# Performance work log

Measured on AMD Instinct MI355X. Metric: run time of the kernel, lower is better.

The kernel has to match this reference:

```python
import jax, jax.numpy as jnp
import numpy as np

B, T, RES, C = 4, 8, 32, 128
TSP, SPLIT = 4, 4
NH_BRANCH = 4  # num_heads // 2 per branch
HID = 4 * C


def layer_norm(x, w, b, eps=1e-5):
    mu = x.mean(-1, keepdims=True)
    var = ((x - mu) ** 2).mean(-1, keepdims=True)
    return (x - mu) * jax.lax.rsqrt(var + eps) * w + b


def dwconv3d(x, w, b):
    # x: (Bw, C, Tsp, Hsp, Wsp); w: (C, 1, 3, 3, 3) depthwise
    y = jax.lax.conv_general_dilated(
        x, w, (1, 1, 1), 'SAME',
        dimension_numbers=('NCDHW', 'OIDHW', 'NCDHW'),
        feature_group_count=x.shape[1])
    return y + b[None, :, None, None, None]


def lepe_attention(q, k, v, conv_w, conv_b, Tsp, Hsp, Wsp, nh, Tt, H, W):
    Bq, L, Cc = q.shape
    hd = Cc // nh
    win = Tsp * Hsp * Wsp
    scale = float(hd) ** -0.5

    def to_win(z):
        z = z.reshape(Bq, Tt // Tsp, Tsp, H // Hsp, Hsp, W // Wsp, Wsp, Cc)
        z = z.transpose(0, 1, 3, 5, 2, 4, 6, 7).reshape(-1, win, nh, hd)
        return z.transpose(0, 2, 1, 3)

    qw = to_win(q) * scale
    kw = to_win(k)
    # v windows as (Bw, C, Tsp, Hsp, Wsp) for the depthwise-conv LePE
    vw5 = v.reshape(Bq, Tt // Tsp, Tsp, H // Hsp, Hsp, W // Wsp, Wsp, Cc)
    vw5 = vw5.transpose(0, 1, 3, 5, 7, 2, 4, 6).reshape(-1, Cc, Tsp, Hsp, Wsp)
    lepe = dwconv3d(vw5, conv_w, conv_b)

    def heads(z5):
        return z5.reshape(-1, nh, hd, win).transpose(0, 1, 3, 2)

    vh, lepeh = heads(vw5), heads(lepe)
    attn = jax.nn.softmax(jnp.einsum('bnqd,bnkd->bnqk', qw, kw), axis=-1)
    out = jnp.einsum('bnqk,bnkd->bnqd', attn, vh) + lepeh
    # windows -> video token order (T, H, W)
    out = out.transpose(0, 2, 1, 3).reshape(
        Bq, Tt // Tsp, H // Hsp, W // Wsp, Tsp, Hsp, Wsp, Cc)
    out = out.transpose(0, 1, 4, 2, 5, 3, 6, 7).reshape(Bq, L, Cc)
    return out


def setup_inputs() -> dict:
    key = jax.random.key(0)
    ks = jax.random.split(key, 16)
    L = T * RES * RES
    h = C // 2
    p = lambda k, s: jax.random.normal(k, s, dtype=jnp.float32) * 0.02
    return {
        'x': jax.random.normal(ks[0], (B, L, C), dtype=jnp.float32),
        'norm1_w': jnp.ones((C,), jnp.float32),
        'norm1_b': jnp.zeros((C,), jnp.float32),
        'qkv_w': p(ks[1], (3 * C, C)),
        'conv_w0': p(ks[2], (h, 1, 3, 3, 3)),
        'conv_b0': jnp.zeros((h,), jnp.float32),
        'conv_w1': p(ks[3], (h, 1, 3, 3, 3)),
        'conv_b1': jnp.zeros((h,), jnp.float32),
        'proj_w': p(ks[4], (C, C)),
        'proj_b': jnp.zeros((C,), jnp.float32),
        'norm2_w': jnp.ones((C,), jnp.float32),
        'norm2_b': jnp.zeros((C,), jnp.float32),
        'fc1_w': p(ks[5], (HID, C)),
        'fc1_b': jnp.zeros((HID,), jnp.float32),
        'fc2_w': p(ks[6], (C, HID)),
        'fc2_b': jnp.zeros((C,), jnp.float32),
    }


def reference(x, norm1_w, norm1_b, qkv_w, conv_w0, conv_b0, conv_w1, conv_b1,
              proj_w, proj_b, norm2_w, norm2_b, fc1_w, fc1_b, fc2_w, fc2_b):
    img = layer_norm(x, norm1_w, norm1_b)
    qkv = img @ qkv_w.T  # (B, L, 3C), split order q, k, v
    q, k, v = jnp.split(qkv, 3, axis=-1)
    h = C // 2
    # branch 0 (idx=0): H_sp = reso, W_sp = split_size
    x1 = lepe_attention(q[..., :h], k[..., :h], v[..., :h], conv_w0, conv_b0,
                        TSP, RES, SPLIT, NH_BRANCH, T, RES, RES)
    # branch 1 (idx=1): H_sp = split_size, W_sp = reso
    x2 = lepe_attention(q[..., h:], k[..., h:], v[..., h:], conv_w1, conv_b1,
                        TSP, SPLIT, RES, NH_BRANCH, T, RES, RES)
    att = jnp.concatenate([x1, x2], axis=2) @ proj_w.T + proj_b
    x = x + att
    y = layer_norm(x, norm2_w, norm2_b)
    y = jax.nn.gelu(y @ fc1_w.T + fc1_b, approximate=False) @ fc2_w.T + fc2_b
    return x + y
```

## Files before the change

### kernel.cpp

```cpp
#include <hip/hip_runtime.h>
#include <math.h>

namespace {
constexpr int C_ = 128;
constexpr int BL = 32768;

typedef __attribute__((ext_vector_type(8))) short bf16x8;
typedef __attribute__((ext_vector_type(4))) float f32x4;
typedef __attribute__((ext_vector_type(4))) _Float16 f16x4;
typedef __attribute__((ext_vector_type(8))) _Float16 f16x8;
typedef __attribute__((ext_vector_type(2))) __fp16 hf2;

__device__ __forceinline__ unsigned short f2bf(float f) {
  unsigned u = __float_as_uint(f);
  return (unsigned short)((u + 0x7fffu + ((u >> 16) & 1u)) >> 16);
}

#if __has_builtin(__builtin_amdgcn_exp2f)
#define EXP2F(x) __builtin_amdgcn_exp2f(x)
#else
#define EXP2F(x) exp2f(x)
#endif
}

__global__ __launch_bounds__(256) void k_cvt(
    const float* __restrict__ qkvw, const float* __restrict__ pw,
    const float* __restrict__ f1w,  const float* __restrict__ f2w,
    const float* __restrict__ cw0,  const float* __restrict__ cw1,
    unsigned short* __restrict__ qkvw_b, unsigned short* __restrict__ pw_b,
    unsigned short* __restrict__ f1w_b,  _Float16* __restrict__ f2w_h,
    float* __restrict__ lepw)
{
  int i = blockIdx.x * 256 + threadIdx.x;
  if (i < 49152)       qkvw_b[i] = f2bf(qkvw[i]);
  else if (i < 65536)  pw_b[i - 49152] = f2bf(pw[i - 49152]);
  else if (i < 131072) f1w_b[i - 65536] = f2bf(f1w[i - 65536]);
  else if (i < 196608) f2w_h[i - 131072] = (_Float16)f2w[i - 131072];
  else if (i < 200064) {
    int j = i - 196608;
    int br = j / 1728, r = j % 1728, widx = r >> 6, ch = r & 63;
    lepw[j] = (br ? cw1 : cw0)[ch * 27 + widx];
  }
}

__global__ __launch_bounds__(256) void k_ln_qkv(
    const float* __restrict__ x,
    const float* __restrict__ nw,
    const float* __restrict__ nb,
    const unsigned short* __restrict__ qkvw_b,
    _Float16* __restrict__ qkv)
{
  __shared__ unsigned short xs[64][136];
  __shared__ unsigned short wbuf[128][136];
  const int tid = threadIdx.x;
  const int row0 = blockIdx.x << 6;

  {
    const int r = tid >> 2, j = tid & 3;
    const float* xp = x + (size_t)(row0 + r) * C_ + j * 32;
    float v[32];
#pragma unroll
    for (int i = 0; i < 8; ++i) {
      float4 u = ((const float4*)xp)[i];
      v[i * 4 + 0] = u.x; v[i * 4 + 1] = u.y; v[i * 4 + 2] = u.z; v[i * 4 + 3] = u.w;
    }
    float s1 = 0.f, s2 = 0.f;
#pragma unroll
    for (int i = 0; i < 32; ++i) { s1 += v[i]; s2 += v[i] * v[i]; }
    s1 += __shfl_down(s1, 2, 4); s1 += __shfl_down(s1, 1, 4);
    s2 += __shfl_down(s2, 2, 4); s2 += __shfl_down(s2, 1, 4);
    float mu = __shfl(s1, 0, 4) * (1.f / 128.f);
    float ms = __shfl(s2, 0, 4) * (1.f / 128.f);
    float rstd = rsqrtf(ms - mu * mu + 1e-5f);
#pragma unroll
    for (int i = 0; i < 8; ++i) {
      ushort4 o;
      int c = j * 32 + i * 4;
      o.x = f2bf((v[i*4+0] - mu) * rstd * nw[c+0] + nb[c+0]);
      o.y = f2bf((v[i*4+1] - mu) * rstd * nw[c+1] + nb[c+1]);
      o.z = f2bf((v[i*4+2] - mu) * rstd * nw[c+2] + nb[c+2]);
      o.w = f2bf((v[i*4+3] - mu) * rstd * nw[c+3] + nb[c+3]);
      *(ushort4*)&xs[r][c] = o;
    }
  }
  __syncthreads();

  const int lane = tid & 63, wave = tid >> 6;
  const int m0 = wave << 4, mi = lane & 15, quad = lane >> 4;

  bf16x8 afr[4];
#pragma unroll
  for (int kt = 0; kt < 4; ++kt)
    afr[kt] = *(const bf16x8*)&xs[m0 + mi][kt * 32 + quad * 8];

  for (int ng = 0; ng < 3; ++ng) {
#pragma unroll
    for (int it = 0; it < 8; ++it) {
      int id = it * 256 + tid;
      int r = id >> 4, c8 = id & 15;
      uint4 u = *(const uint4*)(qkvw_b + (size_t)(ng * 128 + r) * 128 + c8 * 8);
      *(uint4*)&wbuf[r][c8 * 8] = u;
    }
    __syncthreads();

    const float osc = (ng == 0) ? 0.360673762f : 1.0f;
    f32x4 acc[8];
#pragma unroll
    for (int nt = 0; nt < 8; ++nt) acc[nt] = (f32x4){0.f, 0.f, 0.f, 0.f};
#pragma unroll
    for (int nt = 0; nt < 8; ++nt) {
#pragma unroll
      for (int kt = 0; kt < 4; ++kt) {
        bf16x8 bfr = *(const bf16x8*)&wbuf[nt * 16 + mi][kt * 32 + quad * 8];
        acc[nt] = __builtin_amdgcn_mfma_f32_16x16x32_bf16(afr[kt], bfr, acc[nt], 0, 0, 0);
      }
    }
#pragma unroll
    for (int nt = 0; nt < 8; ++nt) {
      int n = (ng * 8 + nt) * 16 + mi;
#pragma unroll
      for (int rr = 0; rr < 4; ++rr) {
        int row = row0 + m0 + quad * 4 + rr;
        qkv[(size_t)row * 384 + n] = (_Float16)(acc[nt][rr] * osc);
      }
    }
    __syncthreads();
  }
}

__global__ __launch_bounds__(512) void k_attn(
    const _Float16* __restrict__ qkv,
    const float* __restrict__ lepw,
    const float* __restrict__ cb0,
    const float* __restrict__ cb1,
    float* __restrict__ attn)
{
  __shared__ _Float16 Ks[512][20];
  __shared__ _Float16 Vs[512][20];

  const int tid = threadIdx.x;
  const int bid = blockIdx.x;
  const int br = bid >> 8, wi = (bid >> 2) & 63, head = bid & 3;
  const int b = wi >> 4, tb = (wi >> 3) & 1, sb = wi & 7;
  const int coff = br * 64 + head * 16;
  const int Hsp = br ? 4 : 32, Wsp = br ? 32 : 4;
  const float* cb = br ? cb1 : cb0;

  auto token_of = [&](int p) -> int {
    int t_in = p >> 7;
    int rem = p & 127;
    int h, w;
    if (br == 0) { h = rem >> 2;            w = sb * 4 + (rem & 3); }
    else         { h = sb * 4 + (rem >> 5); w = rem & 31; }
    return ((b * 8 + tb * 4 + t_in) << 10) + (h << 5) + w;
  };

  {
    const int r = tid;
    const _Float16* base = qkv + (size_t)token_of(r) * 384 + coff;
    f16x8 k0 = *(const f16x8*)(base + 128);
    f16x8 k1 = *(const f16x8*)(base + 136);
    f16x8 v0 = *(const f16x8*)(base + 256);
    f16x8 v1 = *(const f16x8*)(base + 264);
    *(f16x4*)&Ks[r][0]  = (f16x4){k0[0], k0[1], k0[2], k0[3]};
    *(f16x4*)&Ks[r][4]  = (f16x4){k0[4], k0[5], k0[6], k0[7]};
    *(f16x4*)&Ks[r][8]  = (f16x4){k1[0], k1[1], k1[2], k1[3]};
    *(f16x4*)&Ks[r][12] = (f16x4){k1[4], k1[5], k1[6], k1[7]};
    *(f16x4*)&Vs[r][0]  = (f16x4){v0[0], v0[1], v0[2], v0[3]};
    *(f16x4*)&Vs[r][4]  = (f16x4){v0[4], v0[5], v0[6], v0[7]};
    *(f16x4*)&Vs[r][8]  = (f16x4){v1[0], v1[1], v1[2], v1[3]};
    *(f16x4*)&Vs[r][12] = (f16x4){v1[4], v1[5], v1[6], v1[7]};
  }

  const int lane = tid & 63, wave = tid >> 6;
  const int mi = lane & 15, quad = lane >> 4;

  int qtok[4];
  f16x4 qfr[4];
#pragma unroll
  for (int qi = 0; qi < 4; ++qi) {
    qtok[qi] = token_of((wave * 4 + qi) * 16 + mi);
    qfr[qi] = *(const f16x4*)(qkv + (size_t)qtok[qi] * 384 + coff + quad * 4);
  }
  __syncthreads();

  f32x4 acc[4];
  float l[4];
#pragma unroll
  for (int qi = 0; qi < 4; ++qi) { acc[qi] = (f32x4){0.f,0.f,0.f,0.f}; l[qi] = 0.f; }

  const hf2 one2 = {(__fp16)1.f, (__fp16)1.f};

  for (int kt = 0; kt < 32; ++kt) {
    const int kb = kt << 4;
    f16x4 kfr = *(const f16x4*)&Ks[kb + mi][quad * 4];
    f16x4 vfr;
    vfr[0] = Vs[kb + quad * 4 + 0][mi];
    vfr[1] = Vs[kb + quad * 4 + 1][mi];
    vfr[2] = Vs[kb + quad * 4 + 2][mi];
    vfr[3] = Vs[kb + quad * 4 + 3][mi];
#pragma unroll
    for (int qi = 0; qi < 4; ++qi) {
      f32x4 s = __builtin_amdgcn_mfma_f32_16x16x16f16(kfr, qfr[qi], (f32x4){0.f,0.f,0.f,0.f}, 0, 0, 0);
      float p0 = EXP2F(s[0]);
      float p1 = EXP2F(s[1]);
      float p2 = EXP2F(s[2]);
      float p3 = EXP2F(s[3]);
      hf2 plo = __builtin_amdgcn_cvt_pkrtz(p0, p1);
      hf2 phi = __builtin_amdgcn_cvt_pkrtz(p2, p3);
#if __has_builtin(__builtin_amdgcn_fdot2)
      l[qi] = __builtin_amdgcn_fdot2(plo, one2, l[qi], false);
      l[qi] = __builtin_amdgcn_fdot2(phi, one2, l[qi], false);
#else
      l[qi] += (p0 + p1) + (p2 + p3);
#endif
      union { struct { hf2 lo, hi; } h; f16x4 v; } u;
      u.h.lo = plo; u.h.hi = phi;
      acc[qi] = __builtin_amdgcn_mfma_f32_16x16x16f16(vfr, u.v, acc[qi], 0, 0, 0);
    }
  }

#pragma unroll
  for (int qi = 0; qi < 4; ++qi) {
    float lq = l[qi];
    lq += __shfl_xor(lq, 16, 64);
    lq += __shfl_xor(lq, 32, 64);
    float inv = 1.f / lq;

    const int q = (wave * 4 + qi) * 16 + mi;
    int t_in = q >> 7, rem = q & 127;
    int h_in, w_in;
    if (br == 0) { h_in = rem >> 2; w_in = rem & 3; }
    else         { h_in = rem >> 5; w_in = rem & 31; }
    float4 lep = *(const float4*)(cb + head * 16 + quad * 4);
    for (int dz = 0; dz < 3; ++dz) {
      int tz = t_in + dz - 1; if ((unsigned)tz >= 4u) continue;
      for (int dy = 0; dy < 3; ++dy) {
        int ty = h_in + dy - 1; if ((unsigned)ty >= (unsigned)Hsp) continue;
        for (int dx = 0; dx < 3; ++dx) {
          int tx = w_in + dx - 1; if ((unsigned)tx >= (unsigned)Wsp) continue;
          int np = (tz * Hsp + ty) * Wsp + tx;
          int widx = (dz * 3 + dy) * 3 + dx;
          float4 w4 = *(const float4*)(lepw + ((br * 27 + widx) << 6) + head * 16 + quad * 4);
          f16x4 vv = *(const f16x4*)&Vs[np][quad * 4];
          lep.x += w4.x * (float)vv[0];
          lep.y += w4.y * (float)vv[1];
          lep.z += w4.z * (float)vv[2];
          lep.w += w4.w * (float)vv[3];
        }
      }
    }
    float4 o;
    o.x = acc[qi][0] * inv + lep.x;
    o.y = acc[qi][1] * inv + lep.y;
    o.z = acc[qi][2] * inv + lep.z;
    o.w = acc[qi][3] * inv + lep.w;
    *(float4*)(attn + (size_t)qtok[qi] * 128 + coff + quad * 4) = o;
  }
}

__global__ __launch_bounds__(256) void k_proj(
    const float* __restrict__ attn,
    const unsigned short* __restrict__ pw_b,
    const float* __restrict__ pb,
    const float* __restrict__ x,
    float* __restrict__ xr)
{
  __shared__ unsigned short as_[64][136];
  __shared__ unsigned short wbuf[128][136];
  const int tid = threadIdx.x;
  const int row0 = blockIdx.x << 6;

  const float4* ab = (const float4*)(attn + (size_t)row0 * C_);
#pragma unroll
  for (int it = 0; it < 8; ++it) {
    int id = it * 256 + tid;
    float4 u = ab[id];
    int r = id >> 5, c = (id & 31) << 2;
    ushort4 o = { f2bf(u.x), f2bf(u.y), f2bf(u.z), f2bf(u.w) };
    *(ushort4*)&as_[r][c] = o;
  }
#pragma unroll
  for (int it = 0; it < 8; ++it) {
    int id = it * 256 + tid;
    int r = id >> 4, c8 = id & 15;
    uint4 u = *(const uint4*)(pw_b + (size_t)r * 128 + c8 * 8);
    *(uint4*)&wbuf[r][c8 * 8] = u;
  }
  __syncthreads();

  const int lane = tid & 63, wave = tid >> 6;
  const int m0 = wave << 4, mi = lane & 15, quad = lane >> 4;

  bf16x8 afr[4];
#pragma unroll
  for (int kt = 0; kt < 4; ++kt)
    afr[kt] = *(const bf16x8*)&as_[m0 + mi][kt * 32 + quad * 8];

  f32x4 acc[8];
#pragma unroll
  for (int nt = 0; nt < 8; ++nt) acc[nt] = (f32x4){0.f, 0.f, 0.f, 0.f};
#pragma unroll
  for (int nt = 0; nt < 8; ++nt) {
#pragma unroll
    for (int kt = 0; kt < 4; ++kt) {
      bf16x8 bfr = *(const bf16x8*)&wbuf[nt * 16 + mi][kt * 32 + quad * 8];
      acc[nt] = __builtin_amdgcn_mfma_f32_16x16x32_bf16(afr[kt], bfr, acc[nt], 0, 0, 0);
    }
  }
#pragma unroll
  for (int nt = 0; nt < 8; ++nt) {
    int n = nt * 16 + mi;
    float bb = pb[n];
#pragma unroll
    for (int rr = 0; rr < 4; ++rr) {
      int row = row0 + m0 + quad * 4 + rr;
      xr[(size_t)row * C_ + n] = acc[nt][rr] + bb + x[(size_t)row * C_ + n];
    }
  }
}

__global__ __launch_bounds__(256) void k_mlp(
    const float* __restrict__ xr,
    const float* __restrict__ nw,
    const float* __restrict__ nb,
    const unsigned short* __restrict__ f1w_b,
    const float* __restrict__ f1b,
    const _Float16* __restrict__ f2w_h,
    const float* __restrict__ f2b,
    float* __restrict__ out)
{
  __shared__ unsigned short xs[64][136];
  __shared__ unsigned short wbuf[128][136];
  const int tid = threadIdx.x;
  const int row0 = blockIdx.x << 6;

  {
    const int r = tid >> 2, j = tid & 3;
    const float* xp = xr + (size_t)(row0 + r) * C_ + j * 32;
    float v[32];
#pragma unroll
    for (int i = 0; i < 8; ++i) {
      float4 u = ((const float4*)xp)[i];
      v[i*4+0] = u.x; v[i*4+1] = u.y; v[i*4+2] = u.z; v[i*4+3] = u.w;
    }
    float s1 = 0.f, s2 = 0.f;
#pragma unroll
    for (int i = 0; i < 32; ++i) { s1 += v[i]; s2 += v[i] * v[i]; }
    s1 += __shfl_down(s1, 2, 4); s1 += __shfl_down(s1, 1, 4);
    s2 += __shfl_down(s2, 2, 4); s2 += __shfl_down(s2, 1, 4);
    float mu = __shfl(s1, 0, 4) * (1.f / 128.f);
    float ms = __shfl(s2, 0, 4) * (1.f / 128.f);
    float rstd = rsqrtf(ms - mu * mu + 1e-5f);
#pragma unroll
    for (int i = 0; i < 8; ++i) {
      ushort4 o;
      int c = j * 32 + i * 4;
      o.x = f2bf((v[i*4+0] - mu) * rstd * nw[c+0] + nb[c+0]);
      o.y = f2bf((v[i*4+1] - mu) * rstd * nw[c+1] + nb[c+1]);
      o.z = f2bf((v[i*4+2] - mu) * rstd * nw[c+2] + nb[c+2]);
      o.w = f2bf((v[i*4+3] - mu) * rstd * nw[c+3] + nb[c+3]);
      *(ushort4*)&xs[r][c] = o;
    }
  }
  __syncthreads();

  const int lane = tid & 63, wave = tid >> 6;
  const int tok0 = wave << 4, mi = lane & 15, quad = lane >> 4;

  bf16x8 bx[4];
#pragma unroll
  for (int kt = 0; kt < 4; ++kt)
    bx[kt] = *(const bf16x8*)&xs[tok0 + mi][kt * 32 + quad * 8];

  f32x4 oacc[8];
#pragma unroll
  for (int o = 0; o < 8; ++o) oacc[o] = (f32x4){0.f, 0.f, 0.f, 0.f};

  for (int ng = 0; ng < 4; ++ng) {
#pragma unroll
    for (int it = 0; it < 8; ++it) {
      int id = it * 256 + tid;
      int r = id >> 4, c8 = id & 15;
      uint4 u = *(const uint4*)(f1w_b + (size_t)(ng * 128 + r) * 128 + c8 * 8);
      *(uint4*)&wbuf[r][c8 * 8] = u;
    }
    __syncthreads();

    f32x4 hacc[8];
#pragma unroll
    for (int t = 0; t < 8; ++t) hacc[t] = (f32x4){0.f, 0.f, 0.f, 0.f};
#pragma unroll
    for (int t = 0; t < 8; ++t) {
#pragma unroll
      for (int kt = 0; kt < 4; ++kt) {
        bf16x8 wfr = *(const bf16x8*)&wbuf[t * 16 + mi][kt * 32 + quad * 8];
        hacc[t] = __builtin_amdgcn_mfma_f32_16x16x32_bf16(wfr, bx[kt], hacc[t], 0, 0, 0);
      }
    }
    f16x4 ph[8];
#pragma unroll
    for (int t = 0; t < 8; ++t) {
      float4 bj = *(const float4*)(f1b + ng * 128 + t * 16 + quad * 4);
      float h0v = hacc[t][0] + bj.x;
      float h1v = hacc[t][1] + bj.y;
      float h2v = hacc[t][2] + bj.z;
      float h3v = hacc[t][3] + bj.w;
      ph[t][0] = (_Float16)(0.5f * h0v * (1.f + erff(h0v * 0.70710678118654752f)));
      ph[t][1] = (_Float16)(0.5f * h1v * (1.f + erff(h1v * 0.70710678118654752f)));
      ph[t][2] = (_Float16)(0.5f * h2v * (1.f + erff(h2v * 0.70710678118654752f)));
      ph[t][3] = (_Float16)(0.5f * h3v * (1.f + erff(h3v * 0.70710678118654752f)));
    }
    __syncthreads();

#pragma unroll
    for (int it = 0; it < 8; ++it) {
      int id = it * 256 + tid;
      int r = id >> 4, c8 = id & 15;
      uint4 u = *(const uint4*)(f2w_h + (size_t)r * 512 + ng * 128 + c8 * 8);
      *(uint4*)&wbuf[r][c8 * 8] = u;
    }
    __syncthreads();

#pragma unroll
    for (int o = 0; o < 8; ++o) {
#pragma unroll
      for (int t = 0; t < 8; ++t) {
        f16x4 wfr = *(const f16x4*)&wbuf[o * 16 + mi][t * 16 + quad * 4];
        oacc[o] = __builtin_amdgcn_mfma_f32_16x16x16f16(wfr, ph[t], oacc[o], 0, 0, 0);
      }
    }
    __syncthreads();
  }

#pragma unroll
  for (int o = 0; o < 8; ++o) {
    int row = row0 + tok0 + mi;
    int cb4 = o * 16 + quad * 4;
    float4 bo = *(const float4*)(f2b + cb4);
    float4 res = *(const float4*)(xr + (size_t)row * C_ + cb4);
    float4 ov;
    ov.x = oacc[o][0] + bo.x + res.x;
    ov.y = oacc[o][1] + bo.y + res.y;
    ov.z = oacc[o][2] + bo.z + res.z;
    ov.w = oacc[o][3] + bo.w + res.w;
    *(float4*)(out + (size_t)row * C_ + cb4) = ov;
  }
}

extern "C" void kernel_launch(void* const* d_in, const int* in_sizes, int n_in,
                              void* d_out, int out_size, void* d_ws, size_t ws_size,
                              hipStream_t stream)
{
  const float* x    = (const float*)d_in[0];
  const float* n1w  = (const float*)d_in[1];
  const float* n1b  = (const float*)d_in[2];
  const float* qkvw = (const float*)d_in[3];
  const float* cw0  = (const float*)d_in[4];
  const float* cb0  = (const float*)d_in[5];
  const float* cw1  = (const float*)d_in[6];
  const float* cb1  = (const float*)d_in[7];
  const float* pw   = (const float*)d_in[8];
  const float* pb   = (const float*)d_in[9];
  const float* n2w  = (const float*)d_in[10];
  const float* n2b  = (const float*)d_in[11];
  const float* f1w  = (const float*)d_in[12];
  const float* f1b  = (const float*)d_in[13];
  const float* f2w  = (const float*)d_in[14];
  const float* f2b  = (const float*)d_in[15];

  char* ws = (char*)d_ws;
  _Float16* qkv        = (_Float16*)ws;
  float* attn          = (float*)(ws + 25165824);
  float* xr            = (float*)(ws + 41943040);
  unsigned short* qkvw_b = (unsigned short*)(ws + 58720256);
  unsigned short* pw_b   = (unsigned short*)(ws + 58818560);
  unsigned short* f1w_b  = (unsigned short*)(ws + 58851328);
  _Float16*       f2w_h  = (_Float16*)(ws + 58982400);
  float* lepw            = (float*)(ws + 59113472);

  k_cvt   <<<782,     256, 0, stream>>>(qkvw, pw, f1w, f2w, cw0, cw1,
                                        qkvw_b, pw_b, f1w_b, f2w_h, lepw);
  k_ln_qkv<<<BL / 64, 256, 0, stream>>>(x, n1w, n1b, qkvw_b, qkv);
  k_attn  <<<512,     512, 0, stream>>>(qkv, lepw, cb0, cb1, attn);
  k_proj  <<<BL / 64, 256, 0, stream>>>(attn, pw_b, pb, x, xr);
  k_mlp   <<<BL / 64, 256, 0, stream>>>(xr, n2w, n2b, f1w_b, f1b, f2w_h, f2b,
                                        (float*)d_out);
}
```

Measured before the change: 204.0 us.

## Pre-swizzle weights into MFMA fragment order and store window-major fp16 intermediates

Weights are converted once to fp16 in MFMA fragment order, so the GEMM kernels read B fragments straight from global memory instead of staging them through shared memory behind barriers. The QKV kernel now writes Q/K/V in per-head, per-window contiguous layout, which gives the attention kernel coalesced loads in place of token-strided gathers. The attention output and residual intermediates change from fp32 to fp16 to cut memory traffic. In exchange the residual path loses precision (fp16 xr), and all GEMMs switch from bf16 to fp16.

```diff
diff --git a/kernel.cpp b/kernel.cpp
--- a/kernel.cpp
+++ b/kernel.cpp
@@ -5,16 +5,10 @@
 constexpr int C_ = 128;
 constexpr int BL = 32768;
 
-typedef __attribute__((ext_vector_type(8))) short bf16x8;
 typedef __attribute__((ext_vector_type(4))) float f32x4;
 typedef __attribute__((ext_vector_type(4))) _Float16 f16x4;
 typedef __attribute__((ext_vector_type(8))) _Float16 f16x8;
 typedef __attribute__((ext_vector_type(2))) __fp16 hf2;
-
-__device__ __forceinline__ unsigned short f2bf(float f) {
-  unsigned u = __float_as_uint(f);
-  return (unsigned short)((u + 0x7fffu + ((u >> 16) & 1u)) >> 16);
-}
 
 #if __has_builtin(__builtin_amdgcn_exp2f)
 #define EXP2F(x) __builtin_amdgcn_exp2f(x)
@@ -27,16 +21,29 @@
     const float* __restrict__ qkvw, const float* __restrict__ pw,
     const float* __restrict__ f1w,  const float* __restrict__ f2w,
     const float* __restrict__ cw0,  const float* __restrict__ cw1,
-    unsigned short* __restrict__ qkvw_b, unsigned short* __restrict__ pw_b,
-    unsigned short* __restrict__ f1w_b,  _Float16* __restrict__ f2w_h,
+    _Float16* __restrict__ wq, _Float16* __restrict__ wp,
+    _Float16* __restrict__ w1, _Float16* __restrict__ w2,
     float* __restrict__ lepw)
 {
   int i = blockIdx.x * 256 + threadIdx.x;
-  if (i < 49152)       qkvw_b[i] = f2bf(qkvw[i]);
-  else if (i < 65536)  pw_b[i - 49152] = f2bf(pw[i - 49152]);
-  else if (i < 131072) f1w_b[i - 65536] = f2bf(f1w[i - 65536]);
-  else if (i < 196608) f2w_h[i - 131072] = (_Float16)f2w[i - 131072];
-  else if (i < 200064) {
+  if (i < 49152) {
+    int nt = i >> 11, kt = (i >> 9) & 3, l = (i >> 3) & 63, j = i & 7;
+    float v = qkvw[(size_t)(nt * 16 + (l & 15)) * 128 + kt * 32 + (l >> 4) * 8 + j];
+    if (nt < 8) v *= 0.360673762f;
+    wq[i] = (_Float16)v;
+  } else if (i < 65536) {
+    int i2 = i - 49152;
+    int nt = i2 >> 11, kt = (i2 >> 9) & 3, l = (i2 >> 3) & 63, j = i2 & 7;
+    wp[i2] = (_Float16)pw[(size_t)(nt * 16 + (l & 15)) * 128 + kt * 32 + (l >> 4) * 8 + j];
+  } else if (i < 131072) {
+    int i3 = i - 65536;
+    int tg = i3 >> 11, kt = (i3 >> 9) & 3, l = (i3 >> 3) & 63, j = i3 & 7;
+    w1[i3] = (_Float16)f1w[(size_t)(tg * 16 + (l & 15)) * 128 + kt * 32 + (l >> 4) * 8 + j];
+  } else if (i < 196608) {
+    int i4 = i - 131072;
+    int o = i4 >> 13, tg = (i4 >> 8) & 31, l = (i4 >> 2) & 63, j = i4 & 3;
+    w2[i4] = (_Float16)f2w[(size_t)(o * 16 + (l & 15)) * 512 + tg * 16 + (l >> 4) * 4 + j];
+  } else if (i < 200064) {
     int j = i - 196608;
     int br = j / 1728, r = j % 1728, widx = r >> 6, ch = r & 63;
     lepw[j] = (br ? cw1 : cw0)[ch * 27 + widx];
@@ -47,13 +54,15 @@
     const float* __restrict__ x,
     const float* __restrict__ nw,
     const float* __restrict__ nb,
-    const unsigned short* __restrict__ qkvw_b,
-    _Float16* __restrict__ qkv)
-{
-  __shared__ unsigned short xs[64][136];
-  __shared__ unsigned short wbuf[128][136];
+    const _Float16* __restrict__ wq,
+    _Float16* __restrict__ qh, _Float16* __restrict__ kh, _Float16* __restrict__ vh)
+{
+  __shared__ _Float16 xs[64][136];
+  __shared__ _Float16 qt[64][136];
   const int tid = threadIdx.x;
   const int row0 = blockIdx.x << 6;
+  const int bb = row0 >> 13, t = (row0 >> 10) & 7, h0 = (row0 >> 5) & 31;
+  const int tb = t >> 2, t_in = t & 3;
 
   {
     const int r = tid >> 2, j = tid & 3;
@@ -73,14 +82,9 @@
     float ms = __shfl(s2, 0, 4) * (1.f / 128.f);
     float rstd = rsqrtf(ms - mu * mu + 1e-5f);
 #pragma unroll
-    for (int i = 0; i < 8; ++i) {
-      ushort4 o;
-      int c = j * 32 + i * 4;
-      o.x = f2bf((v[i*4+0] - mu) * rstd * nw[c+0] + nb[c+0]);
-      o.y = f2bf((v[i*4+1] - mu) * rstd * nw[c+1] + nb[c+1]);
-      o.z = f2bf((v[i*4+2] - mu) * rstd * nw[c+2] + nb[c+2]);
-      o.w = f2bf((v[i*4+3] - mu) * rstd * nw[c+3] + nb[c+3]);
-      *(ushort4*)&xs[r][c] = o;
+    for (int i = 0; i < 32; ++i) {
+      int c = j * 32 + i;
+      xs[r][c] = (_Float16)((v[i] - mu) * rstd * nw[c] + nb[c]);
     }
   }
   __syncthreads();
@@ -88,52 +92,62 @@
   const int lane = tid & 63, wave = tid >> 6;
   const int m0 = wave << 4, mi = lane & 15, quad = lane >> 4;
 
-  bf16x8 afr[4];
+  f16x8 afr[4];
 #pragma unroll
   for (int kt = 0; kt < 4; ++kt)
-    afr[kt] = *(const bf16x8*)&xs[m0 + mi][kt * 32 + quad * 8];
-
-  for (int ng = 0; ng < 3; ++ng) {
-#pragma unroll
-    for (int it = 0; it < 8; ++it) {
-      int id = it * 256 + tid;
-      int r = id >> 4, c8 = id & 15;
-      uint4 u = *(const uint4*)(qkvw_b + (size_t)(ng * 128 + r) * 128 + c8 * 8);
-      *(uint4*)&wbuf[r][c8 * 8] = u;
-    }
+    afr[kt] = *(const f16x8*)&xs[m0 + mi][kt * 32 + quad * 8];
+
+  for (int g = 0; g < 3; ++g) {
+    f32x4 acc[8];
+#pragma unroll
+    for (int nt = 0; nt < 8; ++nt) acc[nt] = (f32x4){0.f, 0.f, 0.f, 0.f};
+#pragma unroll
+    for (int nt = 0; nt < 8; ++nt) {
+#pragma unroll
+      for (int kt = 0; kt < 4; ++kt) {
+        f16x8 bfr = *(const f16x8*)(wq + ((size_t)(((g * 8 + nt) * 4 + kt) * 64 + lane)) * 8);
+        acc[nt] = __builtin_amdgcn_mfma_f32_16x16x32_f16(afr[kt], bfr, acc[nt], 0, 0, 0);
+      }
+    }
+#pragma unroll
+    for (int nt = 0; nt < 8; ++nt)
+#pragma unroll
+      for (int rr = 0; rr < 4; ++rr)
+        qt[m0 + quad * 4 + rr][nt * 16 + mi] = (_Float16)acc[nt][rr];
     __syncthreads();
 
-    const float osc = (ng == 0) ? 0.360673762f : 1.0f;
-    f32x4 acc[8];
-#pragma unroll
-    for (int nt = 0; nt < 8; ++nt) acc[nt] = (f32x4){0.f, 0.f, 0.f, 0.f};
-#pragma unroll
-    for (int nt = 0; nt < 8; ++nt) {
-#pragma unroll
-      for (int kt = 0; kt < 4; ++kt) {
-        bf16x8 bfr = *(const bf16x8*)&wbuf[nt * 16 + mi][kt * 32 + quad * 8];
-        acc[nt] = __builtin_amdgcn_mfma_f32_16x16x32_bf16(afr[kt], bfr, acc[nt], 0, 0, 0);
+    _Float16* G = (g == 0) ? qh : (g == 1) ? kh : vh;
+#pragma unroll
+    for (int it = 0; it < 4; ++it) {
+      int u = it * 256 + tid;
+      if (u < 512) {
+        int half = u & 1, p = (u >> 1) & 7, head = (u >> 4) & 3, sb = u >> 6;
+        int token = (p >> 2) * 32 + sb * 4 + (p & 3);
+        uint4 d = *(const uint4*)&qt[token][head * 16 + half * 8];
+        int win = bb * 16 + tb * 8 + sb;
+        int pos = t_in * 128 + h0 * 4 + p;
+        *(uint4*)(G + ((size_t)(head * 64 + win) * 512 + pos) * 16 + half * 8) = d;
+      } else {
+        int u2 = u - 512;
+        int half = u2 & 1, pin = (u2 >> 1) & 63, head = u2 >> 7;
+        uint4 d = *(const uint4*)&qt[pin][64 + head * 16 + half * 8];
+        int win = bb * 16 + tb * 8 + (h0 >> 2);
+        int pos = t_in * 128 + (h0 & 3) * 32 + pin;
+        *(uint4*)(G + ((size_t)((4 + head) * 64 + win) * 512 + pos) * 16 + half * 8) = d;
       }
     }
-#pragma unroll
-    for (int nt = 0; nt < 8; ++nt) {
-      int n = (ng * 8 + nt) * 16 + mi;
-#pragma unroll
-      for (int rr = 0; rr < 4; ++rr) {
-        int row = row0 + m0 + quad * 4 + rr;
-        qkv[(size_t)row * 384 + n] = (_Float16)(acc[nt][rr] * osc);
-      }
-    }
     __syncthreads();
   }
 }
 
 __global__ __launch_bounds__(512) void k_attn(
-    const _Float16* __restrict__ qkv,
+    const _Float16* __restrict__ qh,
+    const _Float16* __restrict__ kh,
+    const _Float16* __restrict__ vh,
     const float* __restrict__ lepw,
     const float* __restrict__ cb0,
     const float* __restrict__ cb1,
-    float* __restrict__ attn)
+    _Float16* __restrict__ attnh)
 {
   __shared__ _Float16 Ks[512][20];
   __shared__ _Float16 Vs[512][20];
@@ -145,6 +159,7 @@
   const int coff = br * 64 + head * 16;
   const int Hsp = br ? 4 : 32, Wsp = br ? 32 : 4;
   const float* cb = br ? cb1 : cb0;
+  const size_t base = ((size_t)(br * 4 + head) * 64 + wi) * 512 * 16;
 
   auto token_of = [&](int p) -> int {
     int t_in = p >> 7;
@@ -157,11 +172,12 @@
 
   {
     const int r = tid;
-    const _Float16* base = qkv + (size_t)token_of(r) * 384 + coff;
-    f16x8 k0 = *(const f16x8*)(base + 128);
-    f16x8 k1 = *(const f16x8*)(base + 136);
-    f16x8 v0 = *(const f16x8*)(base + 256);
-    f16x8 v1 = *(const f16x8*)(base + 264);
+    const _Float16* kp = kh + base + r * 16;
+    const _Float16* vp = vh + base + r * 16;
+    f16x8 k0 = *(const f16x8*)kp;
+    f16x8 k1 = *(const f16x8*)(kp + 8);
+    f16x8 v0 = *(const f16x8*)vp;
+    f16x8 v1 = *(const f16x8*)(vp + 8);
     *(f16x4*)&Ks[r][0]  = (f16x4){k0[0], k0[1], k0[2], k0[3]};
     *(f16x4*)&Ks[r][4]  = (f16x4){k0[4], k0[5], k0[6], k0[7]};
     *(f16x4*)&Ks[r][8]  = (f16x4){k1[0], k1[1], k1[2], k1[3]};
@@ -179,8 +195,9 @@
   f16x4 qfr[4];
 #pragma unroll
   for (int qi = 0; qi < 4; ++qi) {
-    qtok[qi] = token_of((wave * 4 + qi) * 16 + mi);
-    qfr[qi] = *(const f16x4*)(qkv + (size_t)qtok[qi] * 384 + coff + quad * 4);
+    int q = (wave * 4 + qi) * 16 + mi;
+    qtok[qi] = token_of(q);
+    qfr[qi] = *(const f16x4*)(qh + base + q * 16 + quad * 4);
   }
   __syncthreads();
 
@@ -250,52 +267,41 @@
         }
       }
     }
-    float4 o;
-    o.x = acc[qi][0] * inv + lep.x;
-    o.y = acc[qi][1] * inv + lep.y;
-    o.z = acc[qi][2] * inv + lep.z;
-    o.w = acc[qi][3] * inv + lep.w;
-    *(float4*)(attn + (size_t)qtok[qi] * 128 + coff + quad * 4) = o;
+    f16x4 ov;
+    ov[0] = (_Float16)(acc[qi][0] * inv + lep.x);
+    ov[1] = (_Float16)(acc[qi][1] * inv + lep.y);
+    ov[2] = (_Float16)(acc[qi][2] * inv + lep.z);
+    ov[3] = (_Float16)(acc[qi][3] * inv + lep.w);
+    *(f16x4*)(attnh + (size_t)qtok[qi] * 128 + coff + quad * 4) = ov;
   }
 }
 
 __global__ __launch_bounds__(256) void k_proj(
-    const float* __restrict__ attn,
-    const unsigned short* __restrict__ pw_b,
+    const _Float16* __restrict__ attnh,
+    const _Float16* __restrict__ wp,
     const float* __restrict__ pb,
     const float* __restrict__ x,
-    float* __restrict__ xr)
-{
-  __shared__ unsigned short as_[64][136];
-  __shared__ unsigned short wbuf[128][136];
+    _Float16* __restrict__ xrh)
+{
+  __shared__ _Float16 as_[64][136];
   const int tid = threadIdx.x;
   const int row0 = blockIdx.x << 6;
 
-  const float4* ab = (const float4*)(attn + (size_t)row0 * C_);
-#pragma unroll
-  for (int it = 0; it < 8; ++it) {
-    int id = it * 256 + tid;
-    float4 u = ab[id];
-    int r = id >> 5, c = (id & 31) << 2;
-    ushort4 o = { f2bf(u.x), f2bf(u.y), f2bf(u.z), f2bf(u.w) };
-    *(ushort4*)&as_[r][c] = o;
-  }
-#pragma unroll
-  for (int it = 0; it < 8; ++it) {
+#pragma unroll
+  for (int it = 0; it < 4; ++it) {
     int id = it * 256 + tid;
     int r = id >> 4, c8 = id & 15;
-    uint4 u = *(const uint4*)(pw_b + (size_t)r * 128 + c8 * 8);
-    *(uint4*)&wbuf[r][c8 * 8] = u;
+    *(uint4*)&as_[r][c8 * 8] = *(const uint4*)(attnh + (size_t)(row0 + r) * 128 + c8 * 8);
   }
   __syncthreads();
 
   const int lane = tid & 63, wave = tid >> 6;
   const int m0 = wave << 4, mi = lane & 15, quad = lane >> 4;
 
-  bf16x8 afr[4];
+  f16x8 afr[4];
 #pragma unroll
   for (int kt = 0; kt < 4; ++kt)
-    afr[kt] = *(const bf16x8*)&as_[m0 + mi][kt * 32 + quad * 8];
+    afr[kt] = *(const f16x8*)&as_[m0 + mi][kt * 32 + quad * 8];
 
   f32x4 acc[8];
 #pragma unroll
@@ -304,45 +310,60 @@
   for (int nt = 0; nt < 8; ++nt) {
 #pragma unroll
     for (int kt = 0; kt < 4; ++kt) {
-      bf16x8 bfr = *(const bf16x8*)&wbuf[nt * 16 + mi][kt * 32 + quad * 8];
-      acc[nt] = __builtin_amdgcn_mfma_f32_16x16x32_bf16(afr[kt], bfr, acc[nt], 0, 0, 0);
-    }
-  }
+      f16x8 bfr = *(const f16x8*)(wp + ((size_t)((nt * 4 + kt) * 64 + lane)) * 8);
+      acc[nt] = __builtin_amdgcn_mfma_f32_16x16x32_f16(afr[kt], bfr, acc[nt], 0, 0, 0);
+    }
+  }
+  __syncthreads();
 #pragma unroll
   for (int nt = 0; nt < 8; ++nt) {
-    int n = nt * 16 + mi;
-    float bb = pb[n];
-#pragma unroll
-    for (int rr = 0; rr < 4; ++rr) {
-      int row = row0 + m0 + quad * 4 + rr;
-      xr[(size_t)row * C_ + n] = acc[nt][rr] + bb + x[(size_t)row * C_ + n];
-    }
+    float bb = pb[nt * 16 + mi];
+#pragma unroll
+    for (int rr = 0; rr < 4; ++rr)
+      as_[m0 + quad * 4 + rr][nt * 16 + mi] = (_Float16)(acc[nt][rr] + bb);
+  }
+  __syncthreads();
+
+#pragma unroll
+  for (int it = 0; it < 4; ++it) {
+    int id = it * 256 + tid;
+    int r = id >> 4, c8 = id & 15;
+    f16x8 v = *(const f16x8*)&as_[r][c8 * 8];
+    const float* xp = x + (size_t)(row0 + r) * 128 + c8 * 8;
+    float4 xa = *(const float4*)xp;
+    float4 xb = *(const float4*)(xp + 4);
+    f16x8 o;
+    o[0] = (_Float16)((float)v[0] + xa.x); o[1] = (_Float16)((float)v[1] + xa.y);
+    o[2] = (_Float16)((float)v[2] + xa.z); o[3] = (_Float16)((float)v[3] + xa.w);
+    o[4] = (_Float16)((float)v[4] + xb.x); o[5] = (_Float16)((float)v[5] + xb.y);
+    o[6] = (_Float16)((float)v[6] + xb.z); o[7] = (_Float16)((float)v[7] + xb.w);
+    *(f16x8*)(xrh + (size_t)(row0 + r) * 128 + c8 * 8) = o;
   }
 }
 
 __global__ __launch_bounds__(256) void k_mlp(
-    const float* __restrict__ xr,
+    const _Float16* __restrict__ xrh,
     const float* __restrict__ nw,
     const float* __restrict__ nb,
-    const unsigned short* __restrict__ f1w_b,
+    const _Float16* __restrict__ w1,
     const float* __restrict__ f1b,
-    const _Float16* __restrict__ f2w_h,
+    const _Float16* __restrict__ w2,
     const float* __restrict__ f2b,
     float* __restrict__ out)
 {
-  __shared__ unsigned short xs[64][136];
-  __shared__ unsigned short wbuf[128][136];
+  __shared__ _Float16 xs[64][136];
   const int tid = threadIdx.x;
   const int row0 = blockIdx.x << 6;
 
   {
     const int r = tid >> 2, j = tid & 3;
-    const float* xp = xr + (size_t)(row0 + r) * C_ + j * 32;
+    const _Float16* xp = xrh + (size_t)(row0 + r) * C_ + j * 32;
     float v[32];
 #pragma unroll
-    for (int i = 0; i < 8; ++i) {
-      float4 u = ((const float4*)xp)[i];
-      v[i*4+0] = u.x; v[i*4+1] = u.y; v[i*4+2] = u.z; v[i*4+3] = u.w;
+    for (int i = 0; i < 4; ++i) {
+      f16x8 u = ((const f16x8*)xp)[i];
+#pragma unroll
+      for (int k = 0; k < 8; ++k) v[i * 8 + k] = (float)u[k];
     }
     float s1 = 0.f, s2 = 0.f;
 #pragma unroll
@@ -353,14 +374,9 @@
     float ms = __shfl(s2, 0, 4) * (1.f / 128.f);
     float rstd = rsqrtf(ms - mu * mu + 1e-5f);
 #pragma unroll
-    for (int i = 0; i < 8; ++i) {
-      ushort4 o;
-      int c = j * 32 + i * 4;
-      o.x = f2bf((v[i*4+0] - mu) * rstd * nw[c+0] + nb[c+0]);
-      o.y = f2bf((v[i*4+1] - mu) * rstd * nw[c+1] + nb[c+1]);
-      o.z = f2bf((v[i*4+2] - mu) * rstd * nw[c+2] + nb[c+2]);
-      o.w = f2bf((v[i*4+3] - mu) * rstd * nw[c+3] + nb[c+3]);
-      *(ushort4*)&xs[r][c] = o;
+    for (int i = 0; i < 32; ++i) {
+      int c = j * 32 + i;
+      xs[r][c] = (_Float16)((v[i] - mu) * rstd * nw[c] + nb[c]);
     }
   }
   __syncthreads();
@@ -368,34 +384,26 @@
   const int lane = tid & 63, wave = tid >> 6;
   const int tok0 = wave << 4, mi = lane & 15, quad = lane >> 4;
 
-  bf16x8 bx[4];
+  f16x8 bx[4];
 #pragma unroll
   for (int kt = 0; kt < 4; ++kt)
-    bx[kt] = *(const bf16x8*)&xs[tok0 + mi][kt * 32 + quad * 8];
+    bx[kt] = *(const f16x8*)&xs[tok0 + mi][kt * 32 + quad * 8];
 
   f32x4 oacc[8];
 #pragma unroll
   for (int o = 0; o < 8; ++o) oacc[o] = (f32x4){0.f, 0.f, 0.f, 0.f};
 
   for (int ng = 0; ng < 4; ++ng) {
-#pragma unroll
-    for (int it = 0; it < 8; ++it) {
-      int id = it * 256 + tid;
-      int r = id >> 4, c8 = id & 15;
-      uint4 u = *(const uint4*)(f1w_b + (size_t)(ng * 128 + r) * 128 + c8 * 8);
-      *(uint4*)&wbuf[r][c8 * 8] = u;
-    }
-    __syncthreads();
-
     f32x4 hacc[8];
 #pragma unroll
     for (int t = 0; t < 8; ++t) hacc[t] = (f32x4){0.f, 0.f, 0.f, 0.f};
 #pragma unroll
     for (int t = 0; t < 8; ++t) {
+      int tg = ng * 8 + t;
 #pragma unroll
       for (int kt = 0; kt < 4; ++kt) {
-        bf16x8 wfr = *(const bf16x8*)&wbuf[t * 16 + mi][kt * 32 + quad * 8];
-        hacc[t] = __builtin_amdgcn_mfma_f32_16x16x32_bf16(wfr, bx[kt], hacc[t], 0, 0, 0);
+        f16x8 wfr = *(const f16x8*)(w1 + ((size_t)((tg * 4 + kt) * 64 + lane)) * 8);
+        hacc[t] = __builtin_amdgcn_mfma_f32_16x16x32_f16(wfr, bx[kt], hacc[t], 0, 0, 0);
       }
     }
     f16x4 ph[8];
@@ -411,26 +419,15 @@
       ph[t][2] = (_Float16)(0.5f * h2v * (1.f + erff(h2v * 0.70710678118654752f)));
       ph[t][3] = (_Float16)(0.5f * h3v * (1.f + erff(h3v * 0.70710678118654752f)));
     }
-    __syncthreads();
-
-#pragma unroll
-    for (int it = 0; it < 8; ++it) {
-      int id = it * 256 + tid;
-      int r = id >> 4, c8 = id & 15;
-      uint4 u = *(const uint4*)(f2w_h + (size_t)r * 512 + ng * 128 + c8 * 8);
-      *(uint4*)&wbuf[r][c8 * 8] = u;
-    }
-    __syncthreads();
-
 #pragma unroll
     for (int o = 0; o < 8; ++o) {
 #pragma unroll
       for (int t = 0; t < 8; ++t) {
-        f16x4 wfr = *(const f16x4*)&wbuf[o * 16 + mi][t * 16 + quad * 4];
+        int tg = ng * 8 + t;
+        f16x4 wfr = *(const f16x4*)(w2 + ((size_t)((o * 32 + tg) * 64 + lane)) * 4);
         oacc[o] = __builtin_amdgcn_mfma_f32_16x16x16f16(wfr, ph[t], oacc[o], 0, 0, 0);
       }
     }
-    __syncthreads();
   }
 
 #pragma unroll
@@ -438,12 +435,12 @@
     int row = row0 + tok0 + mi;
     int cb4 = o * 16 + quad * 4;
     float4 bo = *(const float4*)(f2b + cb4);
-    float4 res = *(const float4*)(xr + (size_t)row * C_ + cb4);
+    f16x4 res = *(const f16x4*)(xrh + (size_t)row * C_ + cb4);
     float4 ov;
-    ov.x = oacc[o][0] + bo.x + res.x;
-    ov.y = oacc[o][1] + bo.y + res.y;
-    ov.z = oacc[o][2] + bo.z + res.z;
-    ov.w = oacc[o][3] + bo.w + res.w;
+    ov.x = oacc[o][0] + bo.x + (float)res[0];
+    ov.y = oacc[o][1] + bo.y + (float)res[1];
+    ov.z = oacc[o][2] + bo.z + (float)res[2];
+    ov.w = oacc[o][3] + bo.w + (float)res[3];
     *(float4*)(out + (size_t)row * C_ + cb4) = ov;
   }
 }
@@ -470,20 +467,22 @@
   const float* f2b  = (const float*)d_in[15];
 
   char* ws = (char*)d_ws;
-  _Float16* qkv        = (_Float16*)ws;
-  float* attn          = (float*)(ws + 25165824);
-  float* xr            = (float*)(ws + 41943040);
-  unsigned short* qkvw_b = (unsigned short*)(ws + 58720256);
-  unsigned short* pw_b   = (unsigned short*)(ws + 58818560);
-  unsigned short* f1w_b  = (unsigned short*)(ws + 58851328);
-  _Float16*       f2w_h  = (_Float16*)(ws + 58982400);
-  float* lepw            = (float*)(ws + 59113472);
+  _Float16* qh    = (_Float16*)ws;
+  _Float16* kh    = (_Float16*)(ws +  8388608);
+  _Float16* vh    = (_Float16*)(ws + 16777216);
+  _Float16* attnh = (_Float16*)(ws + 25165824);
+  _Float16* xrh   = (_Float16*)(ws + 33554432);
+  _Float16* wq    = (_Float16*)(ws + 41943040);
+  _Float16* wp    = (_Float16*)(ws + 42041344);
+  _Float16* w1    = (_Float16*)(ws + 42074112);
+  _Float16* w2    = (_Float16*)(ws + 42205184);
+  float*    lepw  = (float*)   (ws + 42336256);
 
   k_cvt   <<<782,     256, 0, stream>>>(qkvw, pw, f1w, f2w, cw0, cw1,
-                                        qkvw_b, pw_b, f1w_b, f2w_h, lepw);
-  k_ln_qkv<<<BL / 64, 256, 0, stream>>>(x, n1w, n1b, qkvw_b, qkv);
-  k_attn  <<<512,     512, 0, stream>>>(qkv, lepw, cb0, cb1, attn);
-  k_proj  <<<BL / 64, 256, 0, stream>>>(attn, pw_b, pb, x, xr);
-  k_mlp   <<<BL / 64, 256, 0, stream>>>(xr, n2w, n2b, f1w_b, f1b, f2w_h, f2b,
+                                        wq, wp, w1, w2, lepw);
+  k_ln_qkv<<<BL / 64, 256, 0, stream>>>(x, n1w, n1b, wq, qh, kh, vh);
+  k_attn  <<<512,     512, 0, stream>>>(qh, kh, vh, lepw, cb0, cb1, attnh);
+  k_proj  <<<BL / 64, 256, 0, stream>>>(attnh, wp, pb, x, xrh);
+  k_mlp   <<<BL / 64, 256, 0, stream>>>(xrh, n2w, n2b, w1, f1b, w2, f2b,
                                         (float*)d_out);
 }
```

Measured after the change: 237.6 us. 16.4% more time.
